# Performance work log

Measured on AMD Instinct MI355X. Metric: run time of the kernel, lower is better.

Reference implementation:

```python
import jax, jax.numpy as jnp
import numpy as np

N = 8192


def setup_inputs() -> dict:
    key = jax.random.key(0)
    k1, k2, k3, k4, k5, k6 = jax.random.split(key, 6)
    return {
        "thresholds": jax.random.uniform(k1, (N,), dtype=jnp.float32),
        "rules_left": jax.random.randint(k2, (N,), 0, 36, dtype=jnp.int32),
        "rules_right": jax.random.randint(k3, (N,), 0, 36, dtype=jnp.int32),
        "binary_ops": jax.random.randint(k4, (N,), 0, 4, dtype=jnp.int32),
        "left": jax.random.randint(k5, (N,), 0, N, dtype=jnp.int32),
        "right": jax.random.randint(k6, (N,), 0, N, dtype=jnp.int32),
    }


def reference(thresholds, rules_left, rules_right, binary_ops, left, right):
    """DAGGenome.get_active_mask: propagate reachability from node 0 along
    left/right child edges via an N-step scan (faithful to the original)."""
    n = thresholds.shape[0]
    left_valid = (left >= 0) & (left < n)
    right_valid = (right >= 0) & (right < n)
    safe_left = jnp.where(left_valid, left, 0)
    safe_right = jnp.where(right_valid, right, 0)

    def step(reachable, _):
        # scatter: children of currently reachable nodes become reachable
        l = jnp.zeros(n, jnp.bool_).at[safe_left].set(reachable & left_valid)
        r = jnp.zeros(n, jnp.bool_).at[safe_right].set(reachable & right_valid)
        return reachable | l | r, None

    init = jnp.zeros(n, jnp.bool_).at[0].set(True)
    mask, _ = jax.lax.scan(step, init, None, length=n)
    return mask
```

## Files before the change

### kernel.cpp

```cpp
#include <hip/hip_runtime.h>


#define NN  8192
#define NT  1024
#define PER (NN / NT)

__global__ __launch_bounds__(NT) void dag_reach_kernel(
    const int* __restrict__ left,
    const int* __restrict__ right,
    int* __restrict__ out)
{
    __shared__ int   tmp[NN];
    __shared__ short lp16[NN];
    __shared__ short rp16[NN];

    unsigned char* reach   = reinterpret_cast<unsigned char*>(tmp);
    int*           changed = tmp + 2048;

    const int tid = threadIdx.x;

    int lv[PER], rv[PER];
    #pragma unroll
    for (int k = 0; k < PER; ++k) {
        const int i = tid + k * NT;
        lv[k] = left[i];
        rv[k] = right[i];
    }

    #pragma unroll
    for (int k = 0; k < PER; ++k) tmp[tid + k * NT] = -1;
    __syncthreads();
    #pragma unroll
    for (int k = 0; k < PER; ++k) {
        const int i = tid + k * NT;
        const int l = lv[k];
        if (l >= 0 && l < NN) atomicMax(&tmp[l], i);
    }
    __syncthreads();
    #pragma unroll
    for (int k = 0; k < PER; ++k) {
        const int i = tid + k * NT;
        lp16[i] = (short)tmp[i];
    }
    __syncthreads();

    #pragma unroll
    for (int k = 0; k < PER; ++k) tmp[tid + k * NT] = -1;
    __syncthreads();
    #pragma unroll
    for (int k = 0; k < PER; ++k) {
        const int i = tid + k * NT;
        const int r = rv[k];
        if (r >= 0 && r < NN) atomicMax(&tmp[r], i);
    }
    __syncthreads();
    #pragma unroll
    for (int k = 0; k < PER; ++k) {
        const int i = tid + k * NT;
        rp16[i] = (short)tmp[i];
    }
    __syncthreads();

    #pragma unroll
    for (int k = 0; k < PER; ++k) {
        const int i = tid + k * NT;
        reach[i] = (i == 0) ? (unsigned char)1 : (unsigned char)0;
    }
    __syncthreads();

    for (;;) {
        if (tid == 0) *changed = 0;
        __syncthreads();

        int mych = 0;
        #pragma unroll
        for (int k = 0; k < PER; ++k) {
            const int c = tid + k * NT;
            if (!reach[c]) {
                const int a = lp16[c];
                const int b = rp16[c];
                if ((a >= 0 && reach[a]) || (b >= 0 && reach[b])) {
                    reach[c] = 1;
                    mych = 1;
                }
            }
        }
        if (mych) *changed = 1;
        __syncthreads();

        const int done = (*changed == 0);
        __syncthreads();
        if (done) break;
    }

    #pragma unroll
    for (int k = 0; k < PER; ++k) {
        const int i = tid + k * NT;
        out[i] = reach[i] ? 1 : 0;
    }
}

extern "C" void kernel_launch(void* const* d_in, const int* in_sizes, int n_in,
                              void* d_out, int out_size, void* d_ws, size_t ws_size,
                              hipStream_t stream) {
    const int* left  = (const int*)d_in[4];
    const int* right = (const int*)d_in[5];
    int* out = (int*)d_out;

    dag_reach_kernel<<<1, NT, 0, stream>>>(left, right, out);
}
```

Measured before the change: 13.36 us.

## Restructure DAG reachability with blocked ownership, register state, and fused barrier-reduce

Switches to a blocked layout where each thread owns PER consecutive nodes. Parent pointers stay in registers and pending and reached nodes are tracked in per-thread bitmasks. Left and right parent-index atomics are merged into one phase, and the per-iteration changed flag with three barriers becomes a single __syncthreads_or. Each iteration also runs two sweeps so reachability can spread further between barriers. In exchange, shared memory grows (int parent arrays instead of short) and the global loads and stores become strided per thread and less coalesced.

```diff
diff --git a/kernel.cpp b/kernel.cpp
--- a/kernel.cpp
+++ b/kernel.cpp
@@ -10,93 +10,86 @@
     const int* __restrict__ right,
     int* __restrict__ out)
 {
-    __shared__ int   tmp[NN];
-    __shared__ short lp16[NN];
-    __shared__ short rp16[NN];
+    __shared__ int           lpI[NN];
+    __shared__ int           rpI[NN];
+    __shared__ unsigned char reach[NN];
 
-    unsigned char* reach   = reinterpret_cast<unsigned char*>(tmp);
-    int*           changed = tmp + 2048;
+    const int tid  = threadIdx.x;
+    const int base = tid * PER;
 
-    const int tid = threadIdx.x;
+    #pragma unroll
+    for (int k = 0; k < PER; ++k) {
+        lpI[base + k] = -1;
+        rpI[base + k] = -1;
+        reach[base + k] = 0;
+    }
 
     int lv[PER], rv[PER];
     #pragma unroll
     for (int k = 0; k < PER; ++k) {
-        const int i = tid + k * NT;
-        lv[k] = left[i];
-        rv[k] = right[i];
+        lv[k] = left[base + k];
+        rv[k] = right[base + k];
     }
 
-    #pragma unroll
-    for (int k = 0; k < PER; ++k) tmp[tid + k * NT] = -1;
-    __syncthreads();
-    #pragma unroll
-    for (int k = 0; k < PER; ++k) {
-        const int i = tid + k * NT;
-        const int l = lv[k];
-        if (l >= 0 && l < NN) atomicMax(&tmp[l], i);
-    }
-    __syncthreads();
-    #pragma unroll
-    for (int k = 0; k < PER; ++k) {
-        const int i = tid + k * NT;
-        lp16[i] = (short)tmp[i];
-    }
-    __syncthreads();
-
-    #pragma unroll
-    for (int k = 0; k < PER; ++k) tmp[tid + k * NT] = -1;
-    __syncthreads();
-    #pragma unroll
-    for (int k = 0; k < PER; ++k) {
-        const int i = tid + k * NT;
-        const int r = rv[k];
-        if (r >= 0 && r < NN) atomicMax(&tmp[r], i);
-    }
-    __syncthreads();
-    #pragma unroll
-    for (int k = 0; k < PER; ++k) {
-        const int i = tid + k * NT;
-        rp16[i] = (short)tmp[i];
-    }
     __syncthreads();
 
     #pragma unroll
     for (int k = 0; k < PER; ++k) {
-        const int i = tid + k * NT;
-        reach[i] = (i == 0) ? (unsigned char)1 : (unsigned char)0;
+        const int i = base + k;
+        const int l = lv[k];
+        const int r = rv[k];
+        if (l >= 0 && l < NN) atomicMax(&lpI[l], i);
+        if (r >= 0 && r < NN) atomicMax(&rpI[r], i);
     }
+
+    __syncthreads();
+
+    int lp[PER], rp[PER];
+    #pragma unroll
+    for (int k = 0; k < PER; ++k) {
+        lp[k] = lpI[base + k];
+        rp[k] = rpI[base + k];
+    }
+
+    unsigned pend = 0, rmask = 0;
+    #pragma unroll
+    for (int k = 0; k < PER; ++k) {
+        const int c = base + k;
+        if (c == 0) {
+            rmask |= 1u;
+            reach[0] = 1;
+        } else if (lp[k] >= 0 || rp[k] >= 0) {
+            pend |= (1u << k);
+        }
+    }
+
     __syncthreads();
 
     for (;;) {
-        if (tid == 0) *changed = 0;
-        __syncthreads();
-
         int mych = 0;
-        #pragma unroll
-        for (int k = 0; k < PER; ++k) {
-            const int c = tid + k * NT;
-            if (!reach[c]) {
-                const int a = lp16[c];
-                const int b = rp16[c];
-                if ((a >= 0 && reach[a]) || (b >= 0 && reach[b])) {
-                    reach[c] = 1;
-                    mych = 1;
+        for (int sp = 0; sp < 2; ++sp) {
+            #pragma unroll
+            for (int k = 0; k < PER; ++k) {
+                if (pend & (1u << k)) {
+                    const int a = lp[k];
+                    const int b = rp[k];
+                    bool r = (a >= 0) && (reach[a] != 0);
+                    if (!r) r = (b >= 0) && (reach[b] != 0);
+                    if (r) {
+                        reach[base + k] = 1;
+                        rmask |= (1u << k);
+                        pend  &= ~(1u << k);
+                        mych = 1;
+                    }
                 }
             }
         }
-        if (mych) *changed = 1;
-        __syncthreads();
-
-        const int done = (*changed == 0);
-        __syncthreads();
-        if (done) break;
+        if (!__syncthreads_or(mych)) break;
     }
 
     #pragma unroll
     for (int k = 0; k < PER; ++k) {
-        const int i = tid + k * NT;
-        out[i] = reach[i] ? 1 : 0;
+        out[base + k] = (int)((rmask >> k) & 1u);
     }
 }
 
```

After: 15.78 us. 1.18x slower.

## Cut barriers per propagation round and keep parent indices in registers

Applied to the files above, without the earlier changes.

The two separate parent-building passes are merged into one: left and right atomicMax scatters run together. Parent indices are cached in registers, with a sentinel slot standing in for a missing parent, and a per-thread pending bitmask skips nodes that are already settled. A per-epoch flag array replaces the shared 'changed' word, so each round needs one barrier instead of three. The block shrinks to 512 threads and the output is written as vectorized int4 stores. The iteration cap MAXE could cut propagation short on a very deep reachability chain.

```diff
diff --git a/kernel.cpp b/kernel.cpp
--- a/kernel.cpp
+++ b/kernel.cpp
@@ -1,21 +1,21 @@
 #include <hip/hip_runtime.h>
 
 
-#define NN  8192
-#define NT  1024
-#define PER (NN / NT)
+#define NN   8192
+#define NT   512
+#define PER  (NN / NT)
+#define SENT NN
+#define MAXE 512
 
 __global__ __launch_bounds__(NT) void dag_reach_kernel(
     const int* __restrict__ left,
     const int* __restrict__ right,
     int* __restrict__ out)
 {
-    __shared__ int   tmp[NN];
-    __shared__ short lp16[NN];
-    __shared__ short rp16[NN];
-
-    unsigned char* reach   = reinterpret_cast<unsigned char*>(tmp);
-    int*           changed = tmp + 2048;
+    __shared__ int           lpI[NN + 1];
+    __shared__ int           rpI[NN + 1];
+    __shared__ unsigned char reach[NN + 4];
+    __shared__ int           flags[MAXE];
 
     const int tid = threadIdx.x;
 
@@ -28,75 +28,76 @@
     }
 
     #pragma unroll
-    for (int k = 0; k < PER; ++k) tmp[tid + k * NT] = -1;
-    __syncthreads();
-    #pragma unroll
     for (int k = 0; k < PER; ++k) {
         const int i = tid + k * NT;
-        const int l = lv[k];
-        if (l >= 0 && l < NN) atomicMax(&tmp[l], i);
+        lpI[i] = -1;
+        rpI[i] = -1;
     }
-    __syncthreads();
+    int* reach32 = (int*)reach;
     #pragma unroll
-    for (int k = 0; k < PER; ++k) {
-        const int i = tid + k * NT;
-        lp16[i] = (short)tmp[i];
+    for (int k = 0; k < (NN / 4) / NT; ++k)
+        reach32[tid + k * NT] = 0;
+    if (tid == 0) {
+        reach32[NN / 4] = 0;
+        lpI[SENT] = -1;
+        rpI[SENT] = -1;
     }
-    __syncthreads();
-
-    #pragma unroll
-    for (int k = 0; k < PER; ++k) tmp[tid + k * NT] = -1;
-    __syncthreads();
-    #pragma unroll
-    for (int k = 0; k < PER; ++k) {
-        const int i = tid + k * NT;
-        const int r = rv[k];
-        if (r >= 0 && r < NN) atomicMax(&tmp[r], i);
-    }
-    __syncthreads();
-    #pragma unroll
-    for (int k = 0; k < PER; ++k) {
-        const int i = tid + k * NT;
-        rp16[i] = (short)tmp[i];
-    }
+    flags[tid] = 0;
     __syncthreads();
 
     #pragma unroll
     for (int k = 0; k < PER; ++k) {
         const int i = tid + k * NT;
-        reach[i] = (i == 0) ? (unsigned char)1 : (unsigned char)0;
+        const int l = lv[k];
+        const int r = rv[k];
+        if ((unsigned)l < (unsigned)NN) atomicMax(&lpI[l], i);
+        if ((unsigned)r < (unsigned)NN) atomicMax(&rpI[r], i);
     }
     __syncthreads();
 
-    for (;;) {
-        if (tid == 0) *changed = 0;
-        __syncthreads();
+    int lp[PER], rp[PER];
+    unsigned pend = 0;
+    #pragma unroll
+    for (int k = 0; k < PER; ++k) {
+        const int i = tid + k * NT;
+        const int a = lpI[i];
+        const int b = rpI[i];
+        lp[k] = (a < 0) ? SENT : a;
+        rp[k] = (b < 0) ? SENT : b;
+        if ((a >= 0 || b >= 0) && i != 0) pend |= (1u << k);
+    }
+    if (tid == 0) reach[0] = 1;
+    __syncthreads();
 
-        int mych = 0;
-        #pragma unroll
-        for (int k = 0; k < PER; ++k) {
-            const int c = tid + k * NT;
-            if (!reach[c]) {
-                const int a = lp16[c];
-                const int b = rp16[c];
-                if ((a >= 0 && reach[a]) || (b >= 0 && reach[b])) {
-                    reach[c] = 1;
-                    mych = 1;
+    for (int e = 0; ; ++e) {
+        if (pend) {
+            int prog = 0;
+            #pragma unroll
+            for (int k = 0; k < PER; ++k) {
+                if (pend & (1u << k)) {
+                    if (reach[lp[k]] | reach[rp[k]]) {
+                        reach[tid + k * NT] = 1;
+                        pend &= ~(1u << k);
+                        prog = 1;
+                    }
                 }
             }
+            if (prog) flags[e] = 1;
         }
-        if (mych) *changed = 1;
         __syncthreads();
-
-        const int done = (*changed == 0);
-        __syncthreads();
-        if (done) break;
+        if (e >= MAXE - 2 || flags[e] == 0) break;
     }
 
     #pragma unroll
-    for (int k = 0; k < PER; ++k) {
-        const int i = tid + k * NT;
-        out[i] = reach[i] ? 1 : 0;
+    for (int k2 = 0; k2 < (NN / 4) / NT; ++k2) {
+        const int j = tid + k2 * NT;
+        const unsigned w = ((const unsigned*)reach)[j];
+        int4 o;
+        o.x = (int)( w        & 0xffu);
+        o.y = (int)((w >> 8)  & 0xffu);
+        o.z = (int)((w >> 16) & 0xffu);
+        o.w = (int)((w >> 24) & 0xffu);
+        ((int4*)out)[j] = o;
     }
 }
 
```

New measurement: 11.62 us. 13.0% less time.
